# Kernel tuning notes

Hardware: AMD Instinct MI355X
Metric: run time of the kernel (lower is better)

Reference implementation:

```python
import jax, jax.numpy as jnp
import numpy as np

D = 256
NB = 12
B = 2
H = 800
W = 800
KS = [9, 9, 10, 11, 12, 13, 13, 14, 15, 16, 17, 18]
DILS = [1, 1, 1, 1, 2, 2, 2, 2, 3, 3, 3, 3]
STEM_CH = [3, D // 8, D // 4, D // 2, D, D]
STEM_STRIDE = [2, 2, 2, 2, 1]


def gelu(x):
    return jax.nn.gelu(x, approximate=False)


def conv3x3(x, w, b, stride):
    y = jax.lax.conv_general_dilated(x, w, (stride, stride), ((1, 1), (1, 1)),
                                     dimension_numbers=('NCHW', 'OIHW', 'NCHW'))
    return y + b[None, :, None, None]


def group_norm(x, g, be, groups=32, eps=1e-5):
    b, c, h, w = x.shape
    xg = x.reshape(b, groups, c // groups, h, w)
    m = xg.mean((2, 3, 4), keepdims=True)
    v = ((xg - m) ** 2).mean((2, 3, 4), keepdims=True)
    xg = (xg - m) * jax.lax.rsqrt(v + eps)
    return xg.reshape(b, c, h, w) * g[None, :, None, None] + be[None, :, None, None]


def pw(x, w, b, g, be):
    # 1x1 conv + eval-mode BatchNorm (running stats identity -> affine)
    y = jnp.einsum('oc,bcn->bon', w, x)
    if b is not None:
        y = y + b[None, :, None]
    return y * g[None, :, None] + be[None, :, None]


def pos_embed(b, c, h, w):
    # DETR-style normalized 2D sine position embedding -> [b, c, h, w]
    half = c // 2
    scale = 2.0 * np.pi
    ye = jnp.broadcast_to(jnp.arange(1, h + 1, dtype=jnp.float32)[:, None], (h, w)) / h * scale
    xe = jnp.broadcast_to(jnp.arange(1, w + 1, dtype=jnp.float32)[None, :], (h, w)) / w * scale
    dim_t = 10000.0 ** (2.0 * (jnp.arange(half) // 2).astype(jnp.float32) / half)
    px = xe[..., None] / dim_t
    py = ye[..., None] / dim_t
    px = jnp.stack([jnp.sin(px[..., 0::2]), jnp.cos(px[..., 1::2])], -1).reshape(h, w, half)
    py = jnp.stack([jnp.sin(py[..., 0::2]), jnp.cos(py[..., 1::2])], -1).reshape(h, w, half)
    pos = jnp.concatenate([py, px], -1).transpose(2, 0, 1)
    return jnp.broadcast_to(pos[None], (b, c, h, w))


def knn_graph(x, k, dil):
    # x: [B, C, N]; L2-normalize channels, neg squared dist, top-(k*dil), stride by dil
    xn = x * jax.lax.rsqrt(jnp.sum(x * x, 1, keepdims=True) + 1e-12)
    xt = xn.transpose(0, 2, 1)  # [B, N, C]
    sq = jnp.sum(xt * xt, -1)
    neg = 2.0 * jnp.einsum('bnc,bmc->bnm', xt, xt) - sq[:, :, None] - sq[:, None, :]
    _, idx = jax.lax.top_k(neg, k * dil)
    return idx[:, :, ::dil]  # [B, N, k]


def setup_inputs():
    key = jax.random.key(0)
    ks = jax.random.split(key, 16)
    inp = {"x": jax.random.normal(ks[0], (B, 3, H, W), jnp.float32)}
    for i in range(5):
        ci, co = STEM_CH[i], STEM_CH[i + 1]
        inp["sw%d" % i] = jax.random.normal(ks[1 + i], (co, ci, 3, 3), jnp.float32) * 0.05
        inp["sb%d" % i] = jnp.zeros((co,), jnp.float32)
        inp["sg%d" % i] = jnp.ones((co,), jnp.float32)
        inp["sbe%d" % i] = jnp.zeros((co,), jnp.float32)
    s = 0.02
    inp["fc1_w"] = jax.random.normal(ks[6], (NB, D, D), jnp.float32) * s
    inp["fc1_b"] = jnp.zeros((NB, D), jnp.float32)
    inp["fc1_g"] = jnp.ones((NB, D), jnp.float32)
    inp["fc1_be"] = jnp.zeros((NB, D), jnp.float32)
    inp["mr_w"] = jax.random.normal(ks[7], (NB, 2 * D, 2 * D), jnp.float32) * s
    inp["mr_g"] = jnp.ones((NB, 2 * D), jnp.float32)
    inp["mr_be"] = jnp.zeros((NB, 2 * D), jnp.float32)
    inp["fc2_w"] = jax.random.normal(ks[8], (NB, D, 2 * D), jnp.float32) * s
    inp["fc2_b"] = jnp.zeros((NB, D), jnp.float32)
    inp["fc2_g"] = jnp.ones((NB, D), jnp.float32)
    inp["fc2_be"] = jnp.zeros((NB, D), jnp.float32)
    inp["ffn1_w"] = jax.random.normal(ks[9], (NB, 4 * D, D), jnp.float32) * s
    inp["ffn1_b"] = jnp.zeros((NB, 4 * D), jnp.float32)
    inp["ffn1_g"] = jnp.ones((NB, 4 * D), jnp.float32)
    inp["ffn1_be"] = jnp.zeros((NB, 4 * D), jnp.float32)
    inp["ffn2_w"] = jax.random.normal(ks[10], (NB, D, 4 * D), jnp.float32) * s
    inp["ffn2_b"] = jnp.zeros((NB, D), jnp.float32)
    inp["ffn2_g"] = jnp.ones((NB, D), jnp.float32)
    inp["ffn2_be"] = jnp.zeros((NB, D), jnp.float32)
    return inp


def _forward(x, sw0, sb0, sg0, sbe0, sw1, sb1, sg1, sbe1, sw2, sb2, sg2, sbe2,
             sw3, sb3, sg3, sbe3, sw4, sb4, sg4, sbe4,
             fc1_w, fc1_b, fc1_g, fc1_be, mr_w, mr_g, mr_be,
             fc2_w, fc2_b, fc2_g, fc2_be, ffn1_w, ffn1_b, ffn1_g, ffn1_be,
             ffn2_w, ffn2_b, ffn2_g, ffn2_be):
    sws = [sw0, sw1, sw2, sw3, sw4]
    sbs = [sb0, sb1, sb2, sb3, sb4]
    sgs = [sg0, sg1, sg2, sg3, sg4]
    sbes = [sbe0, sbe1, sbe2, sbe3, sbe4]
    for i in range(5):
        x = conv3x3(x, sws[i], sbs[i], STEM_STRIDE[i])
        x = group_norm(x, sgs[i], sbes[i])
        if i < 4:
            x = gelu(x)
    b, c, h, w = x.shape
    x = x + pos_embed(b, c, h, w)
    n = h * w
    x = x.reshape(b, c, n)
    gather = jax.vmap(lambda t, ii: t[ii])  # ([N,C],[N,K]) -> [N,K,C], vmapped over batch
    for i in range(NB):
        # ---- Grapher block ----
        res = x
        hfeat = pw(x, fc1_w[i], fc1_b[i], fc1_g[i], fc1_be[i])  # [b, C, n]
        idx = knn_graph(hfeat, KS[i], DILS[i])                   # [b, n, k]
        ht = hfeat.transpose(0, 2, 1)                            # [b, n, C]
        xj = gather(ht, idx)                                     # [b, n, k, C]
        diff = jnp.max(xj - ht[:, :, None, :], axis=2)           # [b, n, C]
        # channel-interleaved concat: [x0, d0, x1, d1, ...]
        f = jnp.stack([ht, diff], -1).reshape(b, n, 2 * c).transpose(0, 2, 1)
        f = jnp.einsum('oc,bcn->bon', mr_w[i], f)
        f = gelu(f * mr_g[i][None, :, None] + mr_be[i][None, :, None])
        h2 = pw(f, fc2_w[i], fc2_b[i], fc2_g[i], fc2_be[i])
        x = h2 + res
        # ---- FFN block ----
        res = x
        hf = gelu(pw(x, ffn1_w[i], ffn1_b[i], ffn1_g[i], ffn1_be[i]))
        x = pw(hf, ffn2_w[i], ffn2_b[i], ffn2_g[i], ffn2_be[i]) + res
    return x.reshape(b, c, h, w)


def reference(x, sw0, sb0, sg0, sbe0, sw1, sb1, sg1, sbe1, sw2, sb2, sg2, sbe2,
              sw3, sb3, sg3, sbe3, sw4, sb4, sg4, sbe4,
              fc1_w, fc1_b, fc1_g, fc1_be, mr_w, mr_g, mr_be,
              fc2_w, fc2_b, fc2_g, fc2_be, ffn1_w, ffn1_b, ffn1_g, ffn1_be,
              ffn2_w, ffn2_b, ffn2_g, ffn2_be):
    return _forward(x, sw0, sb0, sg0, sbe0, sw1, sb1, sg1, sbe1, sw2, sb2, sg2, sbe2,
                    sw3, sb3, sg3, sbe3, sw4, sb4, sg4, sbe4,
                    fc1_w, fc1_b, fc1_g, fc1_be, mr_w, mr_g, mr_be,
                    fc2_w, fc2_b, fc2_g, fc2_be, ffn1_w, ffn1_b, ffn1_g, ffn1_be,
                    ffn2_w, ffn2_b, ffn2_g, ffn2_be)
```

## Files before the change

kernel.cpp:

```cpp
#include <hip/hip_runtime.h>
#include <math.h>

#define DEVI static __device__ __forceinline__

typedef __attribute__((ext_vector_type(8))) short short8b;
typedef __attribute__((ext_vector_type(4))) float f32x4;

DEVI float gelu_f(float x) { return 0.5f * x * (1.0f + erff(x * 0.70710678118654752440f)); }

DEVI unsigned pack2(float x)
{
    unsigned xb = __float_as_uint(x);
    unsigned hi = (xb + 0x7FFFu + ((xb >> 16) & 1u)) & 0xFFFF0000u;
    float lof = x - __uint_as_float(hi);
    unsigned lb = __float_as_uint(lof);
    unsigned lo = (lb + 0x7FFFu + ((lb >> 16) & 1u)) >> 16;
    return hi | lo;
}
DEVI float unpk(unsigned u)
{
    return __uint_as_float(u & 0xFFFF0000u) + __uint_as_float(u << 16);
}
DEVI unsigned bf16r(float x)
{
    unsigned b = __float_as_uint(x);
    return (b + 0x7FFFu + ((b >> 16) & 1u)) >> 16;
}
DEVI float bf2f(unsigned short u) { return __uint_as_float((unsigned)u << 16); }

DEVI short8b ldfrag(const unsigned* P, int row, int kq)
{
    const unsigned* b = P + row * 18 + kq * 2;
    union { uint2 h[2]; short8b s; } r;
    r.h[0] = *(const uint2*)(b);
    r.h[1] = *(const uint2*)(b + 8);
    return r.s;
}
DEVI void st8(unsigned* b, uint4 v0, uint4 v1)
{
    uint2 t;
    t.x = v0.x; t.y = v0.y; *(uint2*)(b) = t;
    t.x = v0.z; t.y = v0.w; *(uint2*)(b + 2) = t;
    t.x = v1.x; t.y = v1.y; *(uint2*)(b + 4) = t;
    t.x = v1.z; t.y = v1.w; *(uint2*)(b + 6) = t;
}
DEVI void st4(unsigned* b, uint4 v0)
{
    uint2 t;
    t.x = v0.x; t.y = v0.y; *(uint2*)(b) = t;
    t.x = v0.z; t.y = v0.w; *(uint2*)(b + 2) = t;
}

#define MFMA6(ACC, A0, A1, A2F, W0, W1, W2F) do { \
    ACC = __builtin_amdgcn_mfma_f32_16x16x32_bf16(A2F, W0, ACC, 0, 0, 0); \
    ACC = __builtin_amdgcn_mfma_f32_16x16x32_bf16(A0, W2F, ACC, 0, 0, 0); \
    ACC = __builtin_amdgcn_mfma_f32_16x16x32_bf16(A1, W1, ACC, 0, 0, 0); \
    ACC = __builtin_amdgcn_mfma_f32_16x16x32_bf16(A1, W0, ACC, 0, 0, 0); \
    ACC = __builtin_amdgcn_mfma_f32_16x16x32_bf16(A0, W1, ACC, 0, 0, 0); \
    ACC = __builtin_amdgcn_mfma_f32_16x16x32_bf16(A0, W0, ACC, 0, 0, 0); \
} while (0)

template <int CIN, int NCO>
__global__ __launch_bounds__(256)
void conv3x3_t(const float* __restrict__ in, const float* __restrict__ w,
               const float* __restrict__ bias, float* __restrict__ out,
               int Cout, int Hin, int Win, int Hout, int Wout, int stride)
{
    __shared__ __align__(16) float wlds[CIN * 9 * NCO];
    int nsx = gridDim.x, nco = gridDim.y;
    int fid = blockIdx.x + nsx * (blockIdx.y + nco * blockIdx.z);
    int S = nsx * gridDim.z;
    int sPer = S >> 3;
    int k8 = fid & 7, j = fid >> 3;
    int site_inst = k8 + 8 * (j % sPer);
    int co_g = j / sPer;
    int sx = site_inst % nsx;
    int b = site_inst / nsx;

    int co0 = co_g * NCO;
    int tid = threadIdx.x;
    int HWo = Hout * Wout;
    int s = sx * 256 + tid;
    int sc = (s < HWo) ? s : (HWo - 1);
    int ho = sc / Wout, wo = sc % Wout;
    float acc[NCO];
#pragma unroll
    for (int jj = 0; jj < NCO; jj++) acc[jj] = bias[co0 + jj];
    const float* inb = in + (size_t)b * CIN * Hin * Win;
    size_t HWi = (size_t)Hin * Win;

    const int nw = NCO * CIN * 9;
    for (int i = tid; i < nw; i += 256) {
        int jj = i % NCO;
        int rest = i / NCO;
        int ci = rest % CIN, tap = rest / CIN;
        wlds[i] = w[((size_t)(co0 + jj) * CIN + ci) * 9 + tap];
    }
    __syncthreads();
    for (int kh = 0; kh < 3; kh++) {
        int hi = ho * stride - 1 + kh;
        bool okh = (hi >= 0 && hi < Hin);
        for (int kw = 0; kw < 3; kw++) {
            int wi = wo * stride - 1 + kw;
            if (!okh || wi < 0 || wi >= Win) continue;
            int tap = kh * 3 + kw;
            const float* ip = inb + (size_t)hi * Win + wi;
            const float* wp = wlds + (size_t)tap * CIN * NCO;
#pragma unroll 4
            for (int ci = 0; ci < CIN; ci++) {
                float xv = ip[(size_t)ci * HWi];
                const float* wq = wp + ci * NCO;
#pragma unroll
                for (int j4 = 0; j4 < NCO; j4 += 4) {
                    float4 wv = *(const float4*)(wq + j4);
                    acc[j4 + 0] += xv * wv.x; acc[j4 + 1] += xv * wv.y;
                    acc[j4 + 2] += xv * wv.z; acc[j4 + 3] += xv * wv.w;
                }
            }
        }
    }
    if (s < HWo) {
        size_t ob = ((size_t)b * Cout + co0) * HWo + s;
#pragma unroll
        for (int jj = 0; jj < NCO; jj++) out[ob + (size_t)jj * HWo] = acc[jj];
    }
}

__global__ __launch_bounds__(256)
void gn_stats_k(const float* __restrict__ x, double* __restrict__ part,
                int C, int HW, int cpg, int S)
{
    int srt = blockIdx.x, g = blockIdx.y, b = blockIdx.z;
    long len = (long)cpg * HW;
    long chunk = (len + S - 1) / S;
    long lo = (long)srt * chunk;
    long hi = lo + chunk; if (hi > len) hi = len;
    const float* xp = x + ((size_t)b * C + (size_t)g * cpg) * HW;
    double s1 = 0.0, s2 = 0.0;
    for (long i = lo + threadIdx.x; i < hi; i += 256) {
        double v = (double)xp[i];
        s1 += v; s2 += v * v;
    }
    __shared__ double r1[256], r2[256];
    r1[threadIdx.x] = s1; r2[threadIdx.x] = s2;
    __syncthreads();
    for (int t = 128; t > 0; t >>= 1) {
        if (threadIdx.x < t) { r1[threadIdx.x] += r1[threadIdx.x + t]; r2[threadIdx.x] += r2[threadIdx.x + t]; }
        __syncthreads();
    }
    if (threadIdx.x == 0) {
        size_t slot = ((size_t)(b * 32 + g) * S + srt) * 2;
        part[slot] = r1[0];
        part[slot + 1] = r2[0];
    }
}

__global__ __launch_bounds__(64)
void gn_reduce_k(const double* __restrict__ part, float* __restrict__ fin,
                 int S, double cnt)
{
    int t = threadIdx.x;
    double s1 = 0.0, s2 = 0.0;
    for (int s = 0; s < S; s++) {
        size_t slot = ((size_t)t * S + s) * 2;
        s1 += part[slot];
        s2 += part[slot + 1];
    }
    double m = s1 / cnt;
    double var = s2 / cnt - m * m;
    double inv = 1.0 / sqrt(var + 1e-5);
    fin[t * 2] = (float)m;
    fin[t * 2 + 1] = (float)inv;
}

__global__ __launch_bounds__(256)
void gn_apply_k(float* __restrict__ x, const float* __restrict__ fin,
                const float* __restrict__ gma, const float* __restrict__ bta,
                int C, int HW, int cpg, int do_gelu, int total)
{
    int idx = blockIdx.x * 256 + threadIdx.x;
    if (idx >= total) return;
    int c = (idx / HW) % C;
    int b = idx / (HW * C);
    int g = c / cpg;
    float m = fin[(b * 32 + g) * 2];
    float inv = fin[(b * 32 + g) * 2 + 1];
    float v = (x[idx] - m) * inv * gma[c] + bta[c];
    if (do_gelu) v = gelu_f(v);
    x[idx] = v;
}

__global__ __launch_bounds__(256)
void splitT_k(const float* __restrict__ in, unsigned short* __restrict__ P0,
              unsigned short* __restrict__ P1, unsigned short* __restrict__ P2,
              int C, int HW)
{
    __shared__ float tile[64][65];
    int h0 = blockIdx.x * 64, c0 = blockIdx.y * 64, b = blockIdx.z;
    int tid = threadIdx.x;
    int tl = tid & 63;
    const float* inb = in + (size_t)b * C * HW;
#pragma unroll
    for (int p = 0; p < 16; p++) {
        int c = (tid >> 6) + p * 4;
        int h = h0 + tl;
        tile[c][tl] = (h < HW) ? inb[(size_t)(c0 + c) * HW + h] : 0.f;
    }
    __syncthreads();
#pragma unroll
    for (int p = 0; p < 16; p++) {
        int hh = (tid >> 6) + p * 4;
        int h = h0 + hh;
        if (h >= HW) continue;
        int ch = c0 + tl;
        float v = tile[tl][hh];
        unsigned pm = pack2(v);
        size_t off = ((size_t)b * HW + h) * C + ch;
        P0[off] = (unsigned short)(pm >> 16);
        P1[off] = (unsigned short)(pm & 0xFFFFu);
        P2[off] = (unsigned short)bf16r(v - unpk(pm));
    }
}

__global__ __launch_bounds__(256)
void wconvp_k(const float* __restrict__ w, unsigned short* __restrict__ P0,
              unsigned short* __restrict__ P1, unsigned short* __restrict__ P2,
              int Cin, int total)
{
    int idx = blockIdx.x * 256 + threadIdx.x;
    if (idx >= total) return;
    int K = Cin * 9;
    int co = idx / K, k = idx % K;
    int tap = k / Cin, ci = k - tap * Cin;
    float v = w[((size_t)co * Cin + ci) * 9 + tap];
    unsigned pm = pack2(v);
    P0[idx] = (unsigned short)(pm >> 16);
    P1[idx] = (unsigned short)(pm & 0xFFFFu);
    P2[idx] = (unsigned short)bf16r(v - unpk(pm));
}

__global__ __launch_bounds__(256)
void pack5p_k(const float* __restrict__ s0, const float* __restrict__ s1,
              const float* __restrict__ s2, const float* __restrict__ s3,
              const float* __restrict__ s4, unsigned short* __restrict__ P0,
              unsigned short* __restrict__ P1, unsigned short* __restrict__ P2)
{
    int idx = blockIdx.x * 256 + threadIdx.x;
    float v;
    if (idx < 65536)       v = s0[idx];
    else if (idx < 327680) v = s1[idx - 65536];
    else if (idx < 458752) v = s2[idx - 327680];
    else if (idx < 720896) v = s3[idx - 458752];
    else                   v = s4[idx - 720896];
    unsigned pm = pack2(v);
    P0[idx] = (unsigned short)(pm >> 16);
    P1[idx] = (unsigned short)(pm & 0xFFFFu);
    P2[idx] = (unsigned short)bf16r(v - unpk(pm));
}

template <int JT>
__global__ __launch_bounds__(256, 3)
void mgemm6p_k(const unsigned short* __restrict__ A0, const unsigned short* __restrict__ A1,
               const unsigned short* __restrict__ A2,
               const unsigned short* __restrict__ W0, const unsigned short* __restrict__ W1,
               const unsigned short* __restrict__ W2,
               const float* __restrict__ bias, const float* __restrict__ gma,
               const float* __restrict__ bta,
               const unsigned short* __restrict__ R0, const unsigned short* __restrict__ R1,
               const unsigned short* __restrict__ R2,
               unsigned short* __restrict__ C0, unsigned short* __restrict__ C1,
               unsigned short* __restrict__ C2,
               int N, int M, int K, int do_gelu)
{
    const int BM = 32 * JT;
    __shared__ __align__(16) unsigned lA[3][64 * 18];
    __shared__ __align__(16) unsigned lW[3][BM * 18];
    int bz = blockIdx.z;
    int n0 = blockIdx.x * 64, m0 = blockIdx.y * BM;
    int tid = threadIdx.x, wave = tid >> 6, lane = tid & 63;
    int wn = (wave & 1) * 32, wm = (wave >> 1) * (16 * JT);
    int rl = lane & 15, kq = lane >> 4;

    f32x4 acc[2][JT] = {};

    const unsigned* Ag[3] = {(const unsigned*)A0, (const unsigned*)A1, (const unsigned*)A2};
    const unsigned* Wg[3] = {(const unsigned*)W0, (const unsigned*)W1, (const unsigned*)W2};

    int ar = tid >> 2, ah = tid & 3;
    int aga = n0 + ar; if (aga >= N) aga = N - 1;
    size_t abase = (((size_t)bz * N + aga) * K) >> 1;
    unsigned* sA[3];
#pragma unroll
    for (int pl = 0; pl < 3; pl++) sA[pl] = &lA[pl][ar * 18 + ah * 4];

    int wr_ = (JT == 4) ? (tid >> 1) : (tid >> 2);
    int wo_ = (JT == 4) ? ((tid & 1) * 8) : ((tid & 3) * 4);
    size_t wbase = ((size_t)(m0 + wr_) * K) >> 1;
    unsigned* sW[3];
#pragma unroll
    for (int pl = 0; pl < 3; pl++) sW[pl] = &lW[pl][wr_ * 18 + wo_];

    uint4 pa[3], pw[3][2];

#pragma unroll
    for (int pl = 0; pl < 3; pl++) {
        pa[pl] = *(const uint4*)(Ag[pl] + abase + ah * 4);
        const unsigned* h = Wg[pl] + wbase + wo_;
        pw[pl][0] = *(const uint4*)(h);
        if (JT == 4) pw[pl][1] = *(const uint4*)(h + 4);
    }
#pragma unroll
    for (int pl = 0; pl < 3; pl++) {
        st4(sA[pl], pa[pl]);
        if (JT == 4) st8(sW[pl], pw[pl][0], pw[pl][1]); else st4(sW[pl], pw[pl][0]);
    }
    __syncthreads();

    for (int k0 = 0; k0 < K; k0 += 32) {
        bool more = (k0 + 32) < K;
        if (more) {
#pragma unroll
            for (int pl = 0; pl < 3; pl++) {
                pa[pl] = *(const uint4*)(Ag[pl] + abase + ((k0 + 32) >> 1) + ah * 4);
                const unsigned* h = Wg[pl] + wbase + ((k0 + 32) >> 1) + wo_;
                pw[pl][0] = *(const uint4*)(h);
                if (JT == 4) pw[pl][1] = *(const uint4*)(h + 4);
            }
        }
        short8b a0[2], a1[2], a2[2];
#pragma unroll
        for (int i = 0; i < 2; i++) {
            int ra = wn + i * 16 + rl;
            a0[i] = ldfrag(lA[0], ra, kq);
            a1[i] = ldfrag(lA[1], ra, kq);
            a2[i] = ldfrag(lA[2], ra, kq);
        }
        short8b w0[JT], w1[JT], w2[JT];
#pragma unroll
        for (int j = 0; j < JT; j++) {
            int rw = wm + j * 16 + rl;
            w0[j] = ldfrag(lW[0], rw, kq);
            w1[j] = ldfrag(lW[1], rw, kq);
            w2[j] = ldfrag(lW[2], rw, kq);
        }
#pragma unroll
        for (int i = 0; i < 2; i++) {
#pragma unroll
            for (int j = 0; j < JT; j++) {
                MFMA6(acc[i][j], a0[i], a1[i], a2[i], w0[j], w1[j], w2[j]);
            }
        }
        __syncthreads();
        if (more) {
#pragma unroll
            for (int pl = 0; pl < 3; pl++) {
                st4(sA[pl], pa[pl]);
                if (JT == 4) st8(sW[pl], pw[pl][0], pw[pl][1]); else st4(sW[pl], pw[pl][0]);
            }
            __syncthreads();
        }
    }

#pragma unroll
    for (int j = 0; j < JT; j++) {
        int mm = m0 + wm + j * 16 + rl;
        float bs = bias ? bias[mm] : 0.f;
        float gm = gma[mm], bt = bta[mm];
#pragma unroll
        for (int i = 0; i < 2; i++) {
            int tn = n0 + wn + i * 16 + kq * 4;
            f32x4 a = acc[i][j];
#pragma unroll
            for (int r = 0; r < 4; r++) {
                int gn2 = tn + r;
                if (gn2 >= N) continue;
                float v = (a[r] + bs) * gm + bt;
                if (do_gelu) v = gelu_f(v);
                size_t off = ((size_t)bz * N + gn2) * M + mm;
                if (R0) v += (bf2f(R0[off]) + bf2f(R1[off])) + bf2f(R2[off]);
                unsigned pm = pack2(v);
                C0[off] = (unsigned short)(pm >> 16);
                C1[off] = (unsigned short)(pm & 0xFFFFu);
                C2[off] = (unsigned short)bf16r(v - unpk(pm));
            }
        }
    }
}

__global__ __launch_bounds__(256, 3)
void mdist6p_k(const unsigned short* __restrict__ H0, const unsigned short* __restrict__ H1,
               const unsigned short* __restrict__ H2, const float* __restrict__ SQ,
               float* __restrict__ NEG, int Nn, int K, int bz)
{
    __shared__ __align__(16) unsigned lA[3][64 * 18];
    __shared__ __align__(16) unsigned lW[3][64 * 18];
    int q = blockIdx.x;
    int ti = 0;
    while (q >= 40 - ti) { q -= 40 - ti; ti++; }
    int tj = ti + q;
    int i0 = ti * 64, j0 = tj * 64;
    int tid = threadIdx.x, wave = tid >> 6, lane = tid & 63;
    int wn = (wave & 1) * 32, wm = (wave >> 1) * 32;
    int rl = lane & 15, kq = lane >> 4;

    f32x4 acc[2][2] = {};

    const unsigned* Hg[3] = {(const unsigned*)H0, (const unsigned*)H1, (const unsigned*)H2};

    int ar = tid >> 2, ah = tid & 3;
    int gi = i0 + ar; if (gi >= Nn) gi = Nn - 1;
    int gj = j0 + ar; if (gj >= Nn) gj = Nn - 1;
    size_t ibase = (((size_t)bz * Nn + gi) * K) >> 1;
    size_t jbase = (((size_t)bz * Nn + gj) * K) >> 1;
    unsigned* sA[3];
    unsigned* sW[3];
#pragma unroll
    for (int pl = 0; pl < 3; pl++) {
        sA[pl] = &lA[pl][ar * 18 + ah * 4];
        sW[pl] = &lW[pl][ar * 18 + ah * 4];
    }

    uint4 pa[3], pj[3];
#pragma unroll
    for (int pl = 0; pl < 3; pl++) {
        pa[pl] = *(const uint4*)(Hg[pl] + ibase + ah * 4);
        pj[pl] = *(const uint4*)(Hg[pl] + jbase + ah * 4);
    }
#pragma unroll
    for (int pl = 0; pl < 3; pl++) {
        st4(sA[pl], pa[pl]);
        st4(sW[pl], pj[pl]);
    }
    __syncthreads();

    for (int k0 = 0; k0 < K; k0 += 32) {
        bool more = (k0 + 32) < K;
        if (more) {
#pragma unroll
            for (int pl = 0; pl < 3; pl++) {
                pa[pl] = *(const uint4*)(Hg[pl] + ibase + ((k0 + 32) >> 1) + ah * 4);
                pj[pl] = *(const uint4*)(Hg[pl] + jbase + ((k0 + 32) >> 1) + ah * 4);
            }
        }
        short8b a0[2], a1[2], a2[2], w0[2], w1[2], w2[2];
#pragma unroll
        for (int i = 0; i < 2; i++) {
            int ra = wn + i * 16 + rl;
            a0[i] = ldfrag(lA[0], ra, kq);
            a1[i] = ldfrag(lA[1], ra, kq);
            a2[i] = ldfrag(lA[2], ra, kq);
            int rw = wm + i * 16 + rl;
            w0[i] = ldfrag(lW[0], rw, kq);
            w1[i] = ldfrag(lW[1], rw, kq);
            w2[i] = ldfrag(lW[2], rw, kq);
        }
#pragma unroll
        for (int i = 0; i < 2; i++) {
#pragma unroll
            for (int j = 0; j < 2; j++) {
                MFMA6(acc[i][j], a0[i], a1[i], a2[i], w0[j], w1[j], w2[j]);
            }
        }
        __syncthreads();
        if (more) {
#pragma unroll
            for (int pl = 0; pl < 3; pl++) {
                st4(sA[pl], pa[pl]);
                st4(sW[pl], pj[pl]);
            }
            __syncthreads();
        }
    }

    const float* SQb = SQ + (size_t)bz * Nn;
#pragma unroll
    for (int j = 0; j < 2; j++) {
        int nj = j0 + wm + j * 16 + rl;
        if (nj >= Nn) continue;
        float sj = SQb[nj];
#pragma unroll
        for (int i = 0; i < 2; i++) {
            int nio = i0 + wn + i * 16 + kq * 4;
            f32x4 a = acc[i][j];
#pragma unroll
            for (int r = 0; r < 4; r++) {
                int ni = nio + r;
                if (ni >= Nn) continue;
                float d = 2.f * a[r] - SQb[ni] - sj;
                NEG[(size_t)ni * Nn + nj] = d;
                if (i0 != j0) NEG[(size_t)nj * Nn + ni] = d;
            }
        }
    }
}

template <int CIN>
__global__ __launch_bounds__(256, 3)
void mconv6p_k(const unsigned short* __restrict__ T0, const unsigned short* __restrict__ T1,
               const unsigned short* __restrict__ T2,
               const unsigned short* __restrict__ Wc0, const unsigned short* __restrict__ Wc1,
               const unsigned short* __restrict__ Wc2,
               const float* __restrict__ bias, float* __restrict__ out,
               int Cout, int Hin, int Win, int Hout, int Wout, int stride)
{
    const int K = 9 * CIN;
    __shared__ __align__(16) unsigned lA[3][64 * 18];
    __shared__ __align__(16) unsigned lW[3][64 * 18];
    int bz = blockIdx.z;
    int n0 = blockIdx.x * 64, m0 = blockIdx.y * 64;
    int HWo = Hout * Wout;
    int tid = threadIdx.x, wave = tid >> 6, lane = tid & 63;
    int wn = (wave & 1) * 32, wm = (wave >> 1) * 32;
    int rl = lane & 15, kq = lane >> 4;

    f32x4 acc[2][2] = {};

    const unsigned* Tg[3] = {(const unsigned*)T0, (const unsigned*)T1, (const unsigned*)T2};
    const unsigned* Wg[3] = {(const unsigned*)Wc0, (const unsigned*)Wc1, (const unsigned*)Wc2};

    int ar = tid >> 2, ah = tid & 3;
    int s = n0 + ar; if (s >= HWo) s = HWo - 1;
    int ho = s / Wout, wo = s % Wout;
    unsigned* sA[3];
#pragma unroll
    for (int pl = 0; pl < 3; pl++) sA[pl] = &lA[pl][ar * 18 + ah * 4];

    int wr_ = tid >> 2, wo_ = (tid & 3) * 4;
    size_t wbase = ((size_t)(m0 + wr_) * K) >> 1;
    unsigned* sW[3];
#pragma unroll
    for (int pl = 0; pl < 3; pl++) sW[pl] = &lW[pl][wr_ * 18 + wo_];
    size_t HWi = (size_t)Hin * Win;

    uint4 pa[3], pw[3];

    auto loadS = [&](int ks) {
        int kk = ks * 32;
        int tap = kk / CIN;
        int kh = tap / 3, kw = tap % 3;
        int hi = ho * stride - 1 + kh;
        int wi = wo * stride - 1 + kw;
        bool ok = (hi >= 0 && hi < Hin && wi >= 0 && wi < Win);
        if (ok) {
            size_t base = (((size_t)bz * HWi + (size_t)(hi * Win + wi)) * CIN + (kk % CIN)) >> 1;
#pragma unroll
            for (int pl = 0; pl < 3; pl++)
                pa[pl] = *(const uint4*)(Tg[pl] + base + ah * 4);
        } else {
            uint4 z; z.x = 0; z.y = 0; z.z = 0; z.w = 0;
#pragma unroll
            for (int pl = 0; pl < 3; pl++) pa[pl] = z;
        }
#pragma unroll
        for (int pl = 0; pl < 3; pl++)
            pw[pl] = *(const uint4*)(Wg[pl] + wbase + ks * 16 + wo_);
    };
    auto stS = [&]() {
#pragma unroll
        for (int pl = 0; pl < 3; pl++) {
            st4(sA[pl], pa[pl]);
            st4(sW[pl], pw[pl]);
        }
    };

    int nst = K >> 5;
    loadS(0);
    stS();
    __syncthreads();

    for (int ks = 0; ks < nst; ks++) {
        bool more = (ks + 1) < nst;
        if (more) loadS(ks + 1);
        short8b a0[2], a1[2], a2[2];
#pragma unroll
        for (int i = 0; i < 2; i++) {
            int ra = wn + i * 16 + rl;
            a0[i] = ldfrag(lA[0], ra, kq);
            a1[i] = ldfrag(lA[1], ra, kq);
            a2[i] = ldfrag(lA[2], ra, kq);
        }
        short8b w0[2], w1[2], w2[2];
#pragma unroll
        for (int j = 0; j < 2; j++) {
            int rw = wm + j * 16 + rl;
            w0[j] = ldfrag(lW[0], rw, kq);
            w1[j] = ldfrag(lW[1], rw, kq);
            w2[j] = ldfrag(lW[2], rw, kq);
        }
#pragma unroll
        for (int i = 0; i < 2; i++) {
#pragma unroll
            for (int j = 0; j < 2; j++) {
                MFMA6(acc[i][j], a0[i], a1[i], a2[i], w0[j], w1[j], w2[j]);
            }
        }
        __syncthreads();
        if (more) {
            stS();
            __syncthreads();
        }
    }

#pragma unroll
    for (int j = 0; j < 2; j++) {
        int mm = m0 + wm + j * 16 + rl;
        float bs = bias[mm];
#pragma unroll
        for (int i = 0; i < 2; i++) {
            int tn = n0 + wn + i * 16 + kq * 4;
            f32x4 a = acc[i][j];
#pragma unroll
            for (int r = 0; r < 4; r++) {
                int gn2 = tn + r;
                if (gn2 < HWo)
                    out[((size_t)bz * Cout + mm) * HWo + gn2] = a[r] + bs;
            }
        }
    }
}

__global__ __launch_bounds__(256)
void posadd_k(const float* __restrict__ xin, unsigned short* __restrict__ X0,
              unsigned short* __restrict__ X1, unsigned short* __restrict__ X2)
{
    __shared__ float tile[64][65];
    int t0 = blockIdx.x * 64, c0 = blockIdx.y * 64, b = blockIdx.z;
    int tid = threadIdx.x;
    int tl = tid & 63;
    const float* inb = xin + (size_t)b * 256 * 2500;
#pragma unroll
    for (int p = 0; p < 16; p++) {
        int c = (tid >> 6) + p * 4;
        int t = t0 + tl;
        tile[c][tl] = (t < 2500) ? inb[(size_t)(c0 + c) * 2500 + t] : 0.f;
    }
    __syncthreads();
#pragma unroll
    for (int p = 0; p < 16; p++) {
        int tt = (tid >> 6) + p * 4;
        int t = t0 + tt;
        if (t >= 2500) continue;
        int ch = c0 + tl;
        int yy = t / 50, xx = t % 50;
        int cc = ch & 127;
        double v = (double)((ch < 128) ? (yy + 1) : (xx + 1));
        v = v * (6.283185307179586476925287 / 50.0);
        double e = (double)(2 * (cc >> 1)) / 128.0;
        double d = pow(10000.0, e);
        double a = v / d;
        double pp = (cc & 1) ? cos(a) : sin(a);
        float val = tile[tl][tt] + (float)pp;
        size_t off = ((size_t)b * 2500 + t) * 256 + ch;
        unsigned pm = pack2(val);
        X0[off] = (unsigned short)(pm >> 16);
        X1[off] = (unsigned short)(pm & 0xFFFFu);
        X2[off] = (unsigned short)bf16r(val - unpk(pm));
    }
}

__global__ __launch_bounds__(256)
void tok_k(const unsigned short* __restrict__ H0, const unsigned short* __restrict__ H1,
           const unsigned short* __restrict__ H2, unsigned short* __restrict__ T0,
           unsigned short* __restrict__ T1, unsigned short* __restrict__ T2,
           float* __restrict__ SQ)
{
    int wave = threadIdx.x >> 6, lane = threadIdx.x & 63;
    int t = blockIdx.x * 4 + wave;
    int b = blockIdx.y;
    size_t base = ((size_t)b * 2500 + t) * 128;
    const unsigned* h0 = (const unsigned*)H0 + base;
    const unsigned* h1 = (const unsigned*)H1 + base;
    const unsigned* h2 = (const unsigned*)H2 + base;
    float v[4];
    double s = 0.0;
#pragma unroll
    for (int g = 0; g < 2; g++) {
        unsigned ua = h0[lane + g * 64], ub = h1[lane + g * 64], uc = h2[lane + g * 64];
        float lo = (__uint_as_float(ua << 16) + __uint_as_float(ub << 16)) + __uint_as_float(uc << 16);
        float hi = (__uint_as_float(ua & 0xFFFF0000u) + __uint_as_float(ub & 0xFFFF0000u)) + __uint_as_float(uc & 0xFFFF0000u);
        v[2 * g] = lo; v[2 * g + 1] = hi;
        s += (double)lo * lo + (double)hi * hi;
    }
#pragma unroll
    for (int off = 32; off > 0; off >>= 1) s += __shfl_xor(s, off);
    float r = (float)(1.0 / sqrt(s + 1e-12));
    unsigned* t0 = (unsigned*)T0 + base;
    unsigned* t1 = (unsigned*)T1 + base;
    unsigned* t2 = (unsigned*)T2 + base;
    double s2 = 0.0;
#pragma unroll
    for (int g = 0; g < 2; g++) {
        float x0 = v[2 * g] * r, x1 = v[2 * g + 1] * r;
        s2 += (double)x0 * x0 + (double)x1 * x1;
        unsigned p0 = pack2(x0), p1 = pack2(x1);
        t0[lane + g * 64] = (p0 >> 16) | (p1 & 0xFFFF0000u);
        t1[lane + g * 64] = (p0 & 0xFFFFu) | (p1 << 16);
        t2[lane + g * 64] = bf16r(x0 - unpk(p0)) | (bf16r(x1 - unpk(p1)) << 16);
    }
#pragma unroll
    for (int off = 32; off > 0; off >>= 1) s2 += __shfl_xor(s2, off);
    if (lane == 0) SQ[b * 2500 + t] = (float)s2;
}

DEVI unsigned long long pack_key(float x, unsigned idx)
{
    unsigned u = __float_as_uint(x);
    u = (u & 0x80000000u) ? ~u : (u | 0x80000000u);
    return ((unsigned long long)u << 32) | (unsigned long long)(0xFFFFFFFFu - idx);
}

__global__ __launch_bounds__(128)
void topk_k(const float* __restrict__ NEGc, int* __restrict__ IDX,
            int rows, int kd, int dil, int kout, int bz)
{
    __shared__ float vals[2][2560];
    int wave = threadIdx.x >> 6;
    int lane = threadIdx.x & 63;
    int i = blockIdx.x * 2 + wave;
    if (i >= rows) return;
    const float* row = NEGc + (size_t)i * 2500;
    float* v = vals[wave];
    for (int j = lane; j < 2560; j += 64)
        v[j] = (j < 2500) ? (row[j] + 0.0f) : -INFINITY;
    unsigned long long key = pack_key(-INFINITY, 0xFFFFFFFFu);
    for (int q = 0; q < 40; q++) {
        int pos = lane * 40 + q;
        unsigned long long k2 = pack_key(v[pos], (unsigned)pos);
        if (k2 > key) key = k2;
    }
    for (int t = 0; t < kd; t++) {
        unsigned long long r = key;
#pragma unroll
        for (int off = 32; off > 0; off >>= 1) {
            unsigned long long o = __shfl_xor(r, off);
            if (o > r) r = o;
        }
        int sel = (int)(0xFFFFFFFFu - (unsigned)(r & 0xFFFFFFFFull));
        if ((unsigned)sel >= 2500u) sel = 0;
        if (lane == 0 && t % dil == 0)
            IDX[(size_t)(bz * 2500 + i) * kout + t / dil] = sel;
        int lo = sel / 40;
        if (lane == lo) v[sel] = -INFINITY;
        int pos = lo * 40 + lane;
        float x = (lane < 40) ? v[pos] : -INFINITY;
        unsigned long long k2 = pack_key(x, (lane < 40) ? (unsigned)pos : 0xFFFFFFFFu);
#pragma unroll
        for (int off = 32; off > 0; off >>= 1) {
            unsigned long long o = __shfl_xor(k2, off);
            if (o > k2) k2 = o;
        }
        if (lane == lo) key = k2;
    }
}

__global__ __launch_bounds__(256)
void gather_k(const unsigned short* __restrict__ H0, const unsigned short* __restrict__ H1,
              const unsigned short* __restrict__ H2, const int* __restrict__ IDX,
              unsigned short* __restrict__ F0, unsigned short* __restrict__ F1,
              unsigned short* __restrict__ F2, int k)
{
    int t = blockIdx.x;
    int b = blockIdx.y;
    int q = threadIdx.x;
    __shared__ int idx[18];
    if (q < k) {
        int ii = IDX[((size_t)b * 2500 + t) * k + q];
        if ((unsigned)ii >= 2500u) ii = 0;
        idx[q] = ii;
    }
    __syncthreads();
    size_t base = (size_t)b * 2500 * 256;
    size_t co = base + (size_t)t * 256 + q;
    float center = (bf2f(H0[co]) + bf2f(H1[co])) + bf2f(H2[co]);
    float mx = -INFINITY;
    for (int kk = 0; kk < k; kk++) {
        size_t no = base + (size_t)idx[kk] * 256 + q;
        float v = (bf2f(H0[no]) + bf2f(H1[no])) + bf2f(H2[no]);
        mx = fmaxf(mx, v - center);
    }
    unsigned pc = pack2(center), pd = pack2(mx);
    size_t fo = (size_t)b * 2500 * 256 + (size_t)t * 256 + q;
    ((unsigned*)F0)[fo] = (pc >> 16) | (pd & 0xFFFF0000u);
    ((unsigned*)F1)[fo] = (pc & 0xFFFFu) | (pd << 16);
    ((unsigned*)F2)[fo] = bf16r(center - unpk(pc)) | (bf16r(mx - unpk(pd)) << 16);
}

__global__ __launch_bounds__(256)
void outt_k(const unsigned short* __restrict__ X0, const unsigned short* __restrict__ X1,
            const unsigned short* __restrict__ X2, float* __restrict__ out)
{
    __shared__ float tile[64][65];
    int t0 = blockIdx.x * 64, c0 = blockIdx.y * 64, b = blockIdx.z;
    int tid = threadIdx.x;
    int tl = tid & 63;
#pragma unroll
    for (int p = 0; p < 16; p++) {
        int tt = (tid >> 6) + p * 4;
        int t = t0 + tt;
        int tc = (t < 2500) ? t : 2499;
        size_t off = ((size_t)b * 2500 + tc) * 256 + c0 + tl;
        tile[tl][tt] = (bf2f(X0[off]) + bf2f(X1[off])) + bf2f(X2[off]);
    }
    __syncthreads();
#pragma unroll
    for (int p = 0; p < 16; p++) {
        int cc = (tid >> 6) + p * 4;
        int t = t0 + tl;
        if (t < 2500)
            out[((size_t)b * 256 + c0 + cc) * 2500 + t] = tile[cc][tl];
    }
}

extern "C" void kernel_launch(void* const* d_in, const int* in_sizes, int n_in,
                              void* d_out, int out_size, void* d_ws, size_t ws_size,
                              hipStream_t stream)
{
    (void)in_sizes; (void)n_in; (void)out_size; (void)ws_size;
    const float* x_in = (const float*)d_in[0];
    const float *swp[5], *sbp[5], *sgp[5], *sbep[5];
    for (int i = 0; i < 5; i++) {
        swp[i] = (const float*)d_in[1 + 4 * i];
        sbp[i] = (const float*)d_in[2 + 4 * i];
        sgp[i] = (const float*)d_in[3 + 4 * i];
        sbep[i] = (const float*)d_in[4 + 4 * i];
    }
    const float* fc1_w = (const float*)d_in[21];
    const float* fc1_b = (const float*)d_in[22];
    const float* fc1_g = (const float*)d_in[23];
    const float* fc1_be = (const float*)d_in[24];
    const float* mr_w = (const float*)d_in[25];
    const float* mr_g = (const float*)d_in[26];
    const float* mr_be = (const float*)d_in[27];
    const float* fc2_w = (const float*)d_in[28];
    const float* fc2_b = (const float*)d_in[29];
    const float* fc2_g = (const float*)d_in[30];
    const float* fc2_be = (const float*)d_in[31];
    const float* ffn1_w = (const float*)d_in[32];
    const float* ffn1_b = (const float*)d_in[33];
    const float* ffn1_g = (const float*)d_in[34];
    const float* ffn1_be = (const float*)d_in[35];
    const float* ffn2_w = (const float*)d_in[36];
    const float* ffn2_b = (const float*)d_in[37];
    const float* ffn2_g = (const float*)d_in[38];
    const float* ffn2_be = (const float*)d_in[39];

    float* ws = (float*)d_ws;
    const size_t NEG_F = 1920000;
    const size_t G_F   = 3840000;
    const size_t TI_F  = 3000000;
    const size_t CW_F  = 10300000;
    const size_t X_F   = 12500000;
    const size_t HF_F  = 14420000;
    const size_t W_F   = 16340000;
    const size_t SQ_F  = 17815000;
    const size_t PART_F = 17820000;
    const size_t FIN_F = 17829000;
    const size_t IDX_F = 17830000;

    float* ping = ws;
    float* pong = ws + X_F;
    float* NEG  = ws + NEG_F;
    unsigned short* HT0 = (unsigned short*)ws;
    unsigned short* HT1 = HT0 + 1280000;
    unsigned short* HT2 = HT0 + 2560000;
    unsigned short* Fp0 = (unsigned short*)ws;
    unsigned short* Fp1 = Fp0 + 2560000;
    unsigned short* Fp2 = Fp0 + 5120000;
    unsigned short* Gp0 = (unsigned short*)(ws + G_F);
    unsigned short* Gp1 = Gp0 + 2560000;
    unsigned short* Gp2 = Gp0 + 5120000;
    unsigned short* H20 = (unsigned short*)ws;
    unsigned short* H21 = H20 + 5120000;
    unsigned short* H22 = H20 + 10240000;
    unsigned short* TI0 = (unsigned short*)(ws + TI_F);
    unsigned short* CW0 = (unsigned short*)(ws + CW_F);
    unsigned short* X0 = (unsigned short*)(ws + X_F);
    unsigned short* X1 = X0 + 1280000;
    unsigned short* X2 = X0 + 2560000;
    unsigned short* HF0 = (unsigned short*)(ws + HF_F);
    unsigned short* HF1 = HF0 + 1280000;
    unsigned short* HF2b = HF0 + 2560000;
    unsigned short* W0 = (unsigned short*)(ws + W_F);
    unsigned short* W1 = W0 + 983040;
    unsigned short* W2 = W0 + 1966080;
    float* SQ = ws + SQ_F;
    double* PART = (double*)(ws + PART_F);
    float* FIN = ws + FIN_F;
    int* IDX = (int*)(ws + IDX_F);

    int Co[5] = {32, 64, 128, 256, 256};
    int Ho[5] = {400, 200, 100, 50, 50};
    int Ssub[5] = {8, 8, 4, 2, 2};
    float* cur = nullptr;
    for (int l = 0; l < 5; l++) {
        float* outb = (l % 2 == 0) ? ping : pong;
        int HWo = Ho[l] * Ho[l];
        switch (l) {
        case 0:
            conv3x3_t<3, 32><<<dim3(628, 1, 2), 256, 0, stream>>>(
                x_in, swp[0], sbp[0], outb, 32, 800, 800, 400, 400, 2);
            break;
        case 1:
            conv3x3_t<32, 32><<<dim3(160, 2, 2), 256, 0, stream>>>(
                cur, swp[1], sbp[1], outb, 64, 400, 400, 200, 200, 2);
            break;
        case 2:
            conv3x3_t<64, 16><<<dim3(40, 8, 2), 256, 0, stream>>>(
                cur, swp[2], sbp[2], outb, 128, 200, 200, 100, 100, 2);
            break;
        case 3: {
            int psz = 2 * 10000 * 128;
            splitT_k<<<dim3(157, 2, 2), 256, 0, stream>>>(
                cur, TI0, TI0 + psz, TI0 + 2 * psz, 128, 10000);
            int tot = 256 * 1152;
            wconvp_k<<<(tot + 255) / 256, 256, 0, stream>>>(
                swp[3], CW0, CW0 + tot, CW0 + 2 * tot, 128, tot);
            mconv6p_k<128><<<dim3(40, 4, 2), 256, 0, stream>>>(
                TI0, TI0 + psz, TI0 + 2 * psz, CW0, CW0 + tot, CW0 + 2 * tot,
                sbp[3], outb, 256, 100, 100, 50, 50, 2);
            break;
        }
        case 4: {
            int psz = 2 * 2500 * 256;
            splitT_k<<<dim3(40, 4, 2), 256, 0, stream>>>(
                cur, TI0, TI0 + psz, TI0 + 2 * psz, 256, 2500);
            int tot = 256 * 2304;
            wconvp_k<<<(tot + 255) / 256, 256, 0, stream>>>(
                swp[4], CW0, CW0 + tot, CW0 + 2 * tot, 256, tot);
            mconv6p_k<256><<<dim3(40, 4, 2), 256, 0, stream>>>(
                TI0, TI0 + psz, TI0 + 2 * psz, CW0, CW0 + tot, CW0 + 2 * tot,
                sbp[4], outb, 256, 50, 50, 50, 50, 1);
            break;
        }
        }
        int cpg = Co[l] / 32;
        gn_stats_k<<<dim3(Ssub[l], 32, 2), 256, 0, stream>>>(outb, PART, Co[l], HWo, cpg, Ssub[l]);
        gn_reduce_k<<<1, 64, 0, stream>>>(PART, FIN, Ssub[l], (double)cpg * (double)HWo);
        int total = 2 * Co[l] * HWo;
        gn_apply_k<<<(total + 255) / 256, 256, 0, stream>>>(outb, FIN, sgp[l], sbep[l],
                                                            Co[l], HWo, cpg, (l < 4) ? 1 : 0, total);
        cur = outb;
    }
    posadd_k<<<dim3(40, 4, 2), 256, 0, stream>>>(cur, X0, X1, X2);

    const int KS[12] = {9, 9, 10, 11, 12, 13, 13, 14, 15, 16, 17, 18};
    const int DILS[12] = {1, 1, 1, 1, 2, 2, 2, 2, 3, 3, 3, 3};
    const int D = 256, N = 2500;

    for (int i = 0; i < 12; i++) {
        pack5p_k<<<3840, 256, 0, stream>>>(
            fc1_w + (size_t)i * 65536, mr_w + (size_t)i * 262144,
            fc2_w + (size_t)i * 131072, ffn1_w + (size_t)i * 262144,
            ffn2_w + (size_t)i * 262144, W0, W1, W2);

        mgemm6p_k<2><<<dim3(40, 4, 2), 256, 0, stream>>>(
            X0, X1, X2, W0, W1, W2,
            fc1_b + i * D, fc1_g + i * D, fc1_be + i * D,
            nullptr, nullptr, nullptr, HF0, HF1, HF2b, N, D, D, 0);
        tok_k<<<dim3(625, 2), 256, 0, stream>>>(HF0, HF1, HF2b, HT0, HT1, HT2, SQ);
        for (int bz = 0; bz < 2; bz++) {
            mdist6p_k<<<dim3(820, 1, 1), 256, 0, stream>>>(HT0, HT1, HT2, SQ, NEG, N, D, bz);
            topk_k<<<dim3(1250, 1, 1), 128, 0, stream>>>(NEG, IDX, N,
                                                         KS[i] * DILS[i], DILS[i], KS[i], bz);
        }
        gather_k<<<dim3(2500, 2), 256, 0, stream>>>(HF0, HF1, HF2b, IDX, Fp0, Fp1, Fp2, KS[i]);
        mgemm6p_k<4><<<dim3(40, 4, 2), 256, 0, stream>>>(
            Fp0, Fp1, Fp2, W0 + 65536, W1 + 65536, W2 + 65536,
            nullptr, mr_g + i * 512, mr_be + i * 512,
            nullptr, nullptr, nullptr, Gp0, Gp1, Gp2, N, 512, 512, 1);
        mgemm6p_k<2><<<dim3(40, 4, 2), 256, 0, stream>>>(
            Gp0, Gp1, Gp2, W0 + 327680, W1 + 327680, W2 + 327680,
            fc2_b + i * D, fc2_g + i * D, fc2_be + i * D,
            X0, X1, X2, X0, X1, X2, N, D, 512, 0);
        mgemm6p_k<4><<<dim3(40, 8, 2), 256, 0, stream>>>(
            X0, X1, X2, W0 + 458752, W1 + 458752, W2 + 458752,
            ffn1_b + i * 1024, ffn1_g + i * 1024, ffn1_be + i * 1024,
            nullptr, nullptr, nullptr, H20, H21, H22, N, 1024, D, 1);
        mgemm6p_k<2><<<dim3(40, 4, 2), 256, 0, stream>>>(
            H20, H21, H22, W0 + 720896, W1 + 720896, W2 + 720896,
            ffn2_b + i * D, ffn2_g + i * D, ffn2_be + i * D,
            X0, X1, X2, X0, X1, X2, N, D, 1024, 0);
    }

    outt_k<<<dim3(40, 4, 2), 256, 0, stream>>>(X0, X1, X2, (float*)d_out);
}
```

Baseline: 4.390 ms.

## Replace 3-way bf16 split emulation with 2-way fp16 split MFMA

Switches the fp32-emulating matmul scheme from three bf16 planes with six MFMAs per tile to two fp16 planes (hi + residual) with three f16 MFMAs per tile, across the GEMM, distance and conv kernels, and the pack/gather/output helpers. This roughly halves MFMA count, LDS footprint and the global traffic for the split activations and weights. The trade-off is numerical: fp16 has limited exponent range, so large or tiny values may overflow or lose precision, and this could change kNN selection.

```diff
diff --git a/kernel.cpp b/kernel.cpp
--- a/kernel.cpp
+++ b/kernel.cpp
@@ -3,38 +3,34 @@
 
 #define DEVI static __device__ __forceinline__
 
-typedef __attribute__((ext_vector_type(8))) short short8b;
+typedef __attribute__((ext_vector_type(8))) _Float16 half8;
 typedef __attribute__((ext_vector_type(4))) float f32x4;
 
 DEVI float gelu_f(float x) { return 0.5f * x * (1.0f + erff(x * 0.70710678118654752440f)); }
 
-DEVI unsigned pack2(float x)
-{
-    unsigned xb = __float_as_uint(x);
-    unsigned hi = (xb + 0x7FFFu + ((xb >> 16) & 1u)) & 0xFFFF0000u;
-    float lof = x - __uint_as_float(hi);
-    unsigned lb = __float_as_uint(lof);
-    unsigned lo = (lb + 0x7FFFu + ((lb >> 16) & 1u)) >> 16;
-    return hi | lo;
-}
-DEVI float unpk(unsigned u)
-{
-    return __uint_as_float(u & 0xFFFF0000u) + __uint_as_float(u << 16);
-}
-DEVI unsigned bf16r(float x)
-{
-    unsigned b = __float_as_uint(x);
-    return (b + 0x7FFFu + ((b >> 16) & 1u)) >> 16;
-}
-DEVI float bf2f(unsigned short u) { return __uint_as_float((unsigned)u << 16); }
-
-DEVI short8b ldfrag(const unsigned* P, int row, int kq)
+DEVI unsigned short f2h(float x)
+{
+    _Float16 h = (_Float16)x;
+    unsigned short u; __builtin_memcpy(&u, &h, 2); return u;
+}
+DEVI float h2f(unsigned short u)
+{
+    _Float16 h; __builtin_memcpy(&h, &u, 2); return (float)h;
+}
+
+DEVI half8 ldfh(const unsigned* P, int row, int kq)
 {
     const unsigned* b = P + row * 18 + kq * 2;
-    union { uint2 h[2]; short8b s; } r;
+    union { uint2 h[2]; half8 s; } r;
     r.h[0] = *(const uint2*)(b);
     r.h[1] = *(const uint2*)(b + 8);
     return r.s;
+}
+DEVI void st4(unsigned* b, uint4 v0)
+{
+    uint2 t;
+    t.x = v0.x; t.y = v0.y; *(uint2*)(b) = t;
+    t.x = v0.z; t.y = v0.w; *(uint2*)(b + 2) = t;
 }
 DEVI void st8(unsigned* b, uint4 v0, uint4 v1)
 {
@@ -44,20 +40,11 @@
     t.x = v1.x; t.y = v1.y; *(uint2*)(b + 4) = t;
     t.x = v1.z; t.y = v1.w; *(uint2*)(b + 6) = t;
 }
-DEVI void st4(unsigned* b, uint4 v0)
-{
-    uint2 t;
-    t.x = v0.x; t.y = v0.y; *(uint2*)(b) = t;
-    t.x = v0.z; t.y = v0.w; *(uint2*)(b + 2) = t;
-}
-
-#define MFMA6(ACC, A0, A1, A2F, W0, W1, W2F) do { \
-    ACC = __builtin_amdgcn_mfma_f32_16x16x32_bf16(A2F, W0, ACC, 0, 0, 0); \
-    ACC = __builtin_amdgcn_mfma_f32_16x16x32_bf16(A0, W2F, ACC, 0, 0, 0); \
-    ACC = __builtin_amdgcn_mfma_f32_16x16x32_bf16(A1, W1, ACC, 0, 0, 0); \
-    ACC = __builtin_amdgcn_mfma_f32_16x16x32_bf16(A1, W0, ACC, 0, 0, 0); \
-    ACC = __builtin_amdgcn_mfma_f32_16x16x32_bf16(A0, W1, ACC, 0, 0, 0); \
-    ACC = __builtin_amdgcn_mfma_f32_16x16x32_bf16(A0, W0, ACC, 0, 0, 0); \
+
+#define MFMA3(ACC, A0, A1, W0, W1) do { \
+    ACC = __builtin_amdgcn_mfma_f32_16x16x32_f16(A1, W0, ACC, 0, 0, 0); \
+    ACC = __builtin_amdgcn_mfma_f32_16x16x32_f16(A0, W1, ACC, 0, 0, 0); \
+    ACC = __builtin_amdgcn_mfma_f32_16x16x32_f16(A0, W0, ACC, 0, 0, 0); \
 } while (0)
 
 template <int CIN, int NCO>
@@ -192,8 +179,7 @@
 
 __global__ __launch_bounds__(256)
 void splitT_k(const float* __restrict__ in, unsigned short* __restrict__ P0,
-              unsigned short* __restrict__ P1, unsigned short* __restrict__ P2,
-              int C, int HW)
+              unsigned short* __restrict__ P1, int C, int HW)
 {
     __shared__ float tile[64][65];
     int h0 = blockIdx.x * 64, c0 = blockIdx.y * 64, b = blockIdx.z;
@@ -214,18 +200,16 @@
         if (h >= HW) continue;
         int ch = c0 + tl;
         float v = tile[tl][hh];
-        unsigned pm = pack2(v);
+        unsigned short a = f2h(v);
         size_t off = ((size_t)b * HW + h) * C + ch;
-        P0[off] = (unsigned short)(pm >> 16);
-        P1[off] = (unsigned short)(pm & 0xFFFFu);
-        P2[off] = (unsigned short)bf16r(v - unpk(pm));
+        P0[off] = a;
+        P1[off] = f2h(v - h2f(a));
     }
 }
 
 __global__ __launch_bounds__(256)
 void wconvp_k(const float* __restrict__ w, unsigned short* __restrict__ P0,
-              unsigned short* __restrict__ P1, unsigned short* __restrict__ P2,
-              int Cin, int total)
+              unsigned short* __restrict__ P1, int Cin, int total)
 {
     int idx = blockIdx.x * 256 + threadIdx.x;
     if (idx >= total) return;
@@ -233,17 +217,16 @@
     int co = idx / K, k = idx % K;
     int tap = k / Cin, ci = k - tap * Cin;
     float v = w[((size_t)co * Cin + ci) * 9 + tap];
-    unsigned pm = pack2(v);
-    P0[idx] = (unsigned short)(pm >> 16);
-    P1[idx] = (unsigned short)(pm & 0xFFFFu);
-    P2[idx] = (unsigned short)bf16r(v - unpk(pm));
+    unsigned short a = f2h(v);
+    P0[idx] = a;
+    P1[idx] = f2h(v - h2f(a));
 }
 
 __global__ __launch_bounds__(256)
 void pack5p_k(const float* __restrict__ s0, const float* __restrict__ s1,
               const float* __restrict__ s2, const float* __restrict__ s3,
               const float* __restrict__ s4, unsigned short* __restrict__ P0,
-              unsigned short* __restrict__ P1, unsigned short* __restrict__ P2)
+              unsigned short* __restrict__ P1)
 {
     int idx = blockIdx.x * 256 + threadIdx.x;
     float v;
@@ -252,29 +235,24 @@
     else if (idx < 458752) v = s2[idx - 327680];
     else if (idx < 720896) v = s3[idx - 458752];
     else                   v = s4[idx - 720896];
-    unsigned pm = pack2(v);
-    P0[idx] = (unsigned short)(pm >> 16);
-    P1[idx] = (unsigned short)(pm & 0xFFFFu);
-    P2[idx] = (unsigned short)bf16r(v - unpk(pm));
+    unsigned short a = f2h(v);
+    P0[idx] = a;
+    P1[idx] = f2h(v - h2f(a));
 }
 
 template <int JT>
 __global__ __launch_bounds__(256, 3)
-void mgemm6p_k(const unsigned short* __restrict__ A0, const unsigned short* __restrict__ A1,
-               const unsigned short* __restrict__ A2,
+void mgemm3h_k(const unsigned short* __restrict__ A0, const unsigned short* __restrict__ A1,
                const unsigned short* __restrict__ W0, const unsigned short* __restrict__ W1,
-               const unsigned short* __restrict__ W2,
                const float* __restrict__ bias, const float* __restrict__ gma,
                const float* __restrict__ bta,
                const unsigned short* __restrict__ R0, const unsigned short* __restrict__ R1,
-               const unsigned short* __restrict__ R2,
                unsigned short* __restrict__ C0, unsigned short* __restrict__ C1,
-               unsigned short* __restrict__ C2,
                int N, int M, int K, int do_gelu)
 {
     const int BM = 32 * JT;
-    __shared__ __align__(16) unsigned lA[3][64 * 18];
-    __shared__ __align__(16) unsigned lW[3][BM * 18];
+    __shared__ __align__(16) unsigned lA[2][64 * 18];
+    __shared__ __align__(16) unsigned lW[2][BM * 18];
     int bz = blockIdx.z;
     int n0 = blockIdx.x * 64, m0 = blockIdx.y * BM;
     int tid = threadIdx.x, wave = tid >> 6, lane = tid & 63;
@@ -283,34 +261,34 @@
 
     f32x4 acc[2][JT] = {};
 
-    const unsigned* Ag[3] = {(const unsigned*)A0, (const unsigned*)A1, (const unsigned*)A2};
-    const unsigned* Wg[3] = {(const unsigned*)W0, (const unsigned*)W1, (const unsigned*)W2};
+    const unsigned* Ag[2] = {(const unsigned*)A0, (const unsigned*)A1};
+    const unsigned* Wg[2] = {(const unsigned*)W0, (const unsigned*)W1};
 
     int ar = tid >> 2, ah = tid & 3;
     int aga = n0 + ar; if (aga >= N) aga = N - 1;
     size_t abase = (((size_t)bz * N + aga) * K) >> 1;
-    unsigned* sA[3];
-#pragma unroll
-    for (int pl = 0; pl < 3; pl++) sA[pl] = &lA[pl][ar * 18 + ah * 4];
+    unsigned* sA[2];
+#pragma unroll
+    for (int pl = 0; pl < 2; pl++) sA[pl] = &lA[pl][ar * 18 + ah * 4];
 
     int wr_ = (JT == 4) ? (tid >> 1) : (tid >> 2);
     int wo_ = (JT == 4) ? ((tid & 1) * 8) : ((tid & 3) * 4);
     size_t wbase = ((size_t)(m0 + wr_) * K) >> 1;
-    unsigned* sW[3];
-#pragma unroll
-    for (int pl = 0; pl < 3; pl++) sW[pl] = &lW[pl][wr_ * 18 + wo_];
-
-    uint4 pa[3], pw[3][2];
-
-#pragma unroll
-    for (int pl = 0; pl < 3; pl++) {
+    unsigned* sW[2];
+#pragma unroll
+    for (int pl = 0; pl < 2; pl++) sW[pl] = &lW[pl][wr_ * 18 + wo_];
+
+    uint4 pa[2], pw[2][2];
+
+#pragma unroll
+    for (int pl = 0; pl < 2; pl++) {
         pa[pl] = *(const uint4*)(Ag[pl] + abase + ah * 4);
         const unsigned* h = Wg[pl] + wbase + wo_;
         pw[pl][0] = *(const uint4*)(h);
         if (JT == 4) pw[pl][1] = *(const uint4*)(h + 4);
     }
 #pragma unroll
-    for (int pl = 0; pl < 3; pl++) {
+    for (int pl = 0; pl < 2; pl++) {
         st4(sA[pl], pa[pl]);
         if (JT == 4) st8(sW[pl], pw[pl][0], pw[pl][1]); else st4(sW[pl], pw[pl][0]);
     }
@@ -320,40 +298,38 @@
         bool more = (k0 + 32) < K;
         if (more) {
 #pragma unroll
-            for (int pl = 0; pl < 3; pl++) {
+            for (int pl = 0; pl < 2; pl++) {
                 pa[pl] = *(const uint4*)(Ag[pl] + abase + ((k0 + 32) >> 1) + ah * 4);
                 const unsigned* h = Wg[pl] + wbase + ((k0 + 32) >> 1) + wo_;
                 pw[pl][0] = *(const uint4*)(h);
                 if (JT == 4) pw[pl][1] = *(const uint4*)(h + 4);
             }
         }
-        short8b a0[2], a1[2], a2[2];
+        half8 a0[2], a1[2];
 #pragma unroll
         for (int i = 0; i < 2; i++) {
             int ra = wn + i * 16 + rl;
-            a0[i] = ldfrag(lA[0], ra, kq);
-            a1[i] = ldfrag(lA[1], ra, kq);
-            a2[i] = ldfrag(lA[2], ra, kq);
-        }
-        short8b w0[JT], w1[JT], w2[JT];
+            a0[i] = ldfh(lA[0], ra, kq);
+            a1[i] = ldfh(lA[1], ra, kq);
+        }
+        half8 w0[JT], w1[JT];
 #pragma unroll
         for (int j = 0; j < JT; j++) {
             int rw = wm + j * 16 + rl;
-            w0[j] = ldfrag(lW[0], rw, kq);
-            w1[j] = ldfrag(lW[1], rw, kq);
-            w2[j] = ldfrag(lW[2], rw, kq);
+            w0[j] = ldfh(lW[0], rw, kq);
+            w1[j] = ldfh(lW[1], rw, kq);
         }
 #pragma unroll
         for (int i = 0; i < 2; i++) {
 #pragma unroll
             for (int j = 0; j < JT; j++) {
-                MFMA6(acc[i][j], a0[i], a1[i], a2[i], w0[j], w1[j], w2[j]);
+                MFMA3(acc[i][j], a0[i], a1[i], w0[j], w1[j]);
             }
         }
         __syncthreads();
         if (more) {
 #pragma unroll
-            for (int pl = 0; pl < 3; pl++) {
+            for (int pl = 0; pl < 2; pl++) {
                 st4(sA[pl], pa[pl]);
                 if (JT == 4) st8(sW[pl], pw[pl][0], pw[pl][1]); else st4(sW[pl], pw[pl][0]);
             }
@@ -377,23 +353,22 @@
                 float v = (a[r] + bs) * gm + bt;
                 if (do_gelu) v = gelu_f(v);
                 size_t off = ((size_t)bz * N + gn2) * M + mm;
-                if (R0) v += (bf2f(R0[off]) + bf2f(R1[off])) + bf2f(R2[off]);
-                unsigned pm = pack2(v);
-                C0[off] = (unsigned short)(pm >> 16);
-                C1[off] = (unsigned short)(pm & 0xFFFFu);
-                C2[off] = (unsigned short)bf16r(v - unpk(pm));
+                if (R0) v += h2f(R0[off]) + h2f(R1[off]);
+                unsigned short c0 = f2h(v);
+                C0[off] = c0;
+                C1[off] = f2h(v - h2f(c0));
             }
         }
     }
 }
 
 __global__ __launch_bounds__(256, 3)
-void mdist6p_k(const unsigned short* __restrict__ H0, const unsigned short* __restrict__ H1,
-               const unsigned short* __restrict__ H2, const float* __restrict__ SQ,
-               float* __restrict__ NEG, int Nn, int K, int bz)
-{
-    __shared__ __align__(16) unsigned lA[3][64 * 18];
-    __shared__ __align__(16) unsigned lW[3][64 * 18];
+void mdist3h_k(const unsigned short* __restrict__ H0, const unsigned short* __restrict__ H1,
+               const float* __restrict__ SQ, float* __restrict__ NEG,
+               int Nn, int K, int bz)
+{
+    __shared__ __align__(16) unsigned lA[2][64 * 18];
+    __shared__ __align__(16) unsigned lW[2][64 * 18];
     int q = blockIdx.x;
     int ti = 0;
     while (q >= 40 - ti) { q -= 40 - ti; ti++; }
@@ -405,29 +380,29 @@
 
     f32x4 acc[2][2] = {};
 
-    const unsigned* Hg[3] = {(const unsigned*)H0, (const unsigned*)H1, (const unsigned*)H2};
+    const unsigned* Hg[2] = {(const unsigned*)H0, (const unsigned*)H1};
 
     int ar = tid >> 2, ah = tid & 3;
     int gi = i0 + ar; if (gi >= Nn) gi = Nn - 1;
     int gj = j0 + ar; if (gj >= Nn) gj = Nn - 1;
     size_t ibase = (((size_t)bz * Nn + gi) * K) >> 1;
     size_t jbase = (((size_t)bz * Nn + gj) * K) >> 1;
-    unsigned* sA[3];
-    unsigned* sW[3];
-#pragma unroll
-    for (int pl = 0; pl < 3; pl++) {
+    unsigned* sA[2];
+    unsigned* sW[2];
+#pragma unroll
+    for (int pl = 0; pl < 2; pl++) {
         sA[pl] = &lA[pl][ar * 18 + ah * 4];
         sW[pl] = &lW[pl][ar * 18 + ah * 4];
     }
 
-    uint4 pa[3], pj[3];
-#pragma unroll
-    for (int pl = 0; pl < 3; pl++) {
+    uint4 pa[2], pj[2];
+#pragma unroll
+    for (int pl = 0; pl < 2; pl++) {
         pa[pl] = *(const uint4*)(Hg[pl] + ibase + ah * 4);
         pj[pl] = *(const uint4*)(Hg[pl] + jbase + ah * 4);
     }
 #pragma unroll
-    for (int pl = 0; pl < 3; pl++) {
+    for (int pl = 0; pl < 2; pl++) {
         st4(sA[pl], pa[pl]);
         st4(sW[pl], pj[pl]);
     }
@@ -437,34 +412,32 @@
         bool more = (k0 + 32) < K;
         if (more) {
 #pragma unroll
-            for (int pl = 0; pl < 3; pl++) {
+            for (int pl = 0; pl < 2; pl++) {
                 pa[pl] = *(const uint4*)(Hg[pl] + ibase + ((k0 + 32) >> 1) + ah * 4);
                 pj[pl] = *(const uint4*)(Hg[pl] + jbase + ((k0 + 32) >> 1) + ah * 4);
             }
         }
-        short8b a0[2], a1[2], a2[2], w0[2], w1[2], w2[2];
+        half8 a0[2], a1[2], w0[2], w1[2];
 #pragma unroll
         for (int i = 0; i < 2; i++) {
             int ra = wn + i * 16 + rl;
-            a0[i] = ldfrag(lA[0], ra, kq);
-            a1[i] = ldfrag(lA[1], ra, kq);
-            a2[i] = ldfrag(lA[2], ra, kq);
+            a0[i] = ldfh(lA[0], ra, kq);
+            a1[i] = ldfh(lA[1], ra, kq);
             int rw = wm + i * 16 + rl;
-            w0[i] = ldfrag(lW[0], rw, kq);
-            w1[i] = ldfrag(lW[1], rw, kq);
-            w2[i] = ldfrag(lW[2], rw, kq);
+            w0[i] = ldfh(lW[0], rw, kq);
+            w1[i] = ldfh(lW[1], rw, kq);
         }
 #pragma unroll
         for (int i = 0; i < 2; i++) {
 #pragma unroll
             for (int j = 0; j < 2; j++) {
-                MFMA6(acc[i][j], a0[i], a1[i], a2[i], w0[j], w1[j], w2[j]);
+                MFMA3(acc[i][j], a0[i], a1[i], w0[j], w1[j]);
             }
         }
         __syncthreads();
         if (more) {
 #pragma unroll
-            for (int pl = 0; pl < 3; pl++) {
+            for (int pl = 0; pl < 2; pl++) {
                 st4(sA[pl], pa[pl]);
                 st4(sW[pl], pj[pl]);
             }
@@ -496,16 +469,14 @@
 
 template <int CIN>
 __global__ __launch_bounds__(256, 3)
-void mconv6p_k(const unsigned short* __restrict__ T0, const unsigned short* __restrict__ T1,
-               const unsigned short* __restrict__ T2,
+void mconv3h_k(const unsigned short* __restrict__ T0, const unsigned short* __restrict__ T1,
                const unsigned short* __restrict__ Wc0, const unsigned short* __restrict__ Wc1,
-               const unsigned short* __restrict__ Wc2,
                const float* __restrict__ bias, float* __restrict__ out,
                int Cout, int Hin, int Win, int Hout, int Wout, int stride)
 {
     const int K = 9 * CIN;
-    __shared__ __align__(16) unsigned lA[3][64 * 18];
-    __shared__ __align__(16) unsigned lW[3][64 * 18];
+    __shared__ __align__(16) unsigned lA[2][64 * 18];
+    __shared__ __align__(16) unsigned lW[2][64 * 18];
     int bz = blockIdx.z;
     int n0 = blockIdx.x * 64, m0 = blockIdx.y * 64;
     int HWo = Hout * Wout;
@@ -515,24 +486,24 @@
 
     f32x4 acc[2][2] = {};
 
-    const unsigned* Tg[3] = {(const unsigned*)T0, (const unsigned*)T1, (const unsigned*)T2};
-    const unsigned* Wg[3] = {(const unsigned*)Wc0, (const unsigned*)Wc1, (const unsigned*)Wc2};
+    const unsigned* Tg[2] = {(const unsigned*)T0, (const unsigned*)T1};
+    const unsigned* Wg[2] = {(const unsigned*)Wc0, (const unsigned*)Wc1};
 
     int ar = tid >> 2, ah = tid & 3;
     int s = n0 + ar; if (s >= HWo) s = HWo - 1;
     int ho = s / Wout, wo = s % Wout;
-    unsigned* sA[3];
-#pragma unroll
-    for (int pl = 0; pl < 3; pl++) sA[pl] = &lA[pl][ar * 18 + ah * 4];
+    unsigned* sA[2];
+#pragma unroll
+    for (int pl = 0; pl < 2; pl++) sA[pl] = &lA[pl][ar * 18 + ah * 4];
 
     int wr_ = tid >> 2, wo_ = (tid & 3) * 4;
     size_t wbase = ((size_t)(m0 + wr_) * K) >> 1;
-    unsigned* sW[3];
-#pragma unroll
-    for (int pl = 0; pl < 3; pl++) sW[pl] = &lW[pl][wr_ * 18 + wo_];
+    unsigned* sW[2];
+#pragma unroll
+    for (int pl = 0; pl < 2; pl++) sW[pl] = &lW[pl][wr_ * 18 + wo_];
     size_t HWi = (size_t)Hin * Win;
 
-    uint4 pa[3], pw[3];
+    uint4 pa[2], pw[2];
 
     auto loadS = [&](int ks) {
         int kk = ks * 32;
@@ -544,20 +515,20 @@
         if (ok) {
             size_t base = (((size_t)bz * HWi + (size_t)(hi * Win + wi)) * CIN + (kk % CIN)) >> 1;
 #pragma unroll
-            for (int pl = 0; pl < 3; pl++)
+            for (int pl = 0; pl < 2; pl++)
                 pa[pl] = *(const uint4*)(Tg[pl] + base + ah * 4);
         } else {
             uint4 z; z.x = 0; z.y = 0; z.z = 0; z.w = 0;
 #pragma unroll
-            for (int pl = 0; pl < 3; pl++) pa[pl] = z;
-        }
-#pragma unroll
-        for (int pl = 0; pl < 3; pl++)
+            for (int pl = 0; pl < 2; pl++) pa[pl] = z;
+        }
+#pragma unroll
+        for (int pl = 0; pl < 2; pl++)
             pw[pl] = *(const uint4*)(Wg[pl] + wbase + ks * 16 + wo_);
     };
     auto stS = [&]() {
 #pragma unroll
-        for (int pl = 0; pl < 3; pl++) {
+        for (int pl = 0; pl < 2; pl++) {
             st4(sA[pl], pa[pl]);
             st4(sW[pl], pw[pl]);
         }
@@ -571,27 +542,25 @@
     for (int ks = 0; ks < nst; ks++) {
         bool more = (ks + 1) < nst;
         if (more) loadS(ks + 1);
-        short8b a0[2], a1[2], a2[2];
+        half8 a0[2], a1[2];
 #pragma unroll
         for (int i = 0; i < 2; i++) {
             int ra = wn + i * 16 + rl;
-            a0[i] = ldfrag(lA[0], ra, kq);
-            a1[i] = ldfrag(lA[1], ra, kq);
-            a2[i] = ldfrag(lA[2], ra, kq);
-        }
-        short8b w0[2], w1[2], w2[2];
+            a0[i] = ldfh(lA[0], ra, kq);
+            a1[i] = ldfh(lA[1], ra, kq);
+        }
+        half8 w0[2], w1[2];
 #pragma unroll
         for (int j = 0; j < 2; j++) {
             int rw = wm + j * 16 + rl;
-            w0[j] = ldfrag(lW[0], rw, kq);
-            w1[j] = ldfrag(lW[1], rw, kq);
-            w2[j] = ldfrag(lW[2], rw, kq);
+            w0[j] = ldfh(lW[0], rw, kq);
+            w1[j] = ldfh(lW[1], rw, kq);
         }
 #pragma unroll
         for (int i = 0; i < 2; i++) {
 #pragma unroll
             for (int j = 0; j < 2; j++) {
-                MFMA6(acc[i][j], a0[i], a1[i], a2[i], w0[j], w1[j], w2[j]);
+                MFMA3(acc[i][j], a0[i], a1[i], w0[j], w1[j]);
             }
         }
         __syncthreads();
@@ -621,7 +590,7 @@
 
 __global__ __launch_bounds__(256)
 void posadd_k(const float* __restrict__ xin, unsigned short* __restrict__ X0,
-              unsigned short* __restrict__ X1, unsigned short* __restrict__ X2)
+              unsigned short* __restrict__ X1)
 {
     __shared__ float tile[64][65];
     int t0 = blockIdx.x * 64, c0 = blockIdx.y * 64, b = blockIdx.z;
@@ -651,17 +620,15 @@
         double pp = (cc & 1) ? cos(a) : sin(a);
         float val = tile[tl][tt] + (float)pp;
         size_t off = ((size_t)b * 2500 + t) * 256 + ch;
-        unsigned pm = pack2(val);
-        X0[off] = (unsigned short)(pm >> 16);
-        X1[off] = (unsigned short)(pm & 0xFFFFu);
-        X2[off] = (unsigned short)bf16r(val - unpk(pm));
+        unsigned short a0 = f2h(val);
+        X0[off] = a0;
+        X1[off] = f2h(val - h2f(a0));
     }
 }
 
 __global__ __launch_bounds__(256)
 void tok_k(const unsigned short* __restrict__ H0, const unsigned short* __restrict__ H1,
-           const unsigned short* __restrict__ H2, unsigned short* __restrict__ T0,
-           unsigned short* __restrict__ T1, unsigned short* __restrict__ T2,
+           unsigned short* __restrict__ T0, unsigned short* __restrict__ T1,
            float* __restrict__ SQ)
 {
     int wave = threadIdx.x >> 6, lane = threadIdx.x & 63;
@@ -670,14 +637,13 @@
     size_t base = ((size_t)b * 2500 + t) * 128;
     const unsigned* h0 = (const unsigned*)H0 + base;
     const unsigned* h1 = (const unsigned*)H1 + base;
-    const unsigned* h2 = (const unsigned*)H2 + base;
     float v[4];
     double s = 0.0;
 #pragma unroll
     for (int g = 0; g < 2; g++) {
-        unsigned ua = h0[lane + g * 64], ub = h1[lane + g * 64], uc = h2[lane + g * 64];
-        float lo = (__uint_as_float(ua << 16) + __uint_as_float(ub << 16)) + __uint_as_float(uc << 16);
-        float hi = (__uint_as_float(ua & 0xFFFF0000u) + __uint_as_float(ub & 0xFFFF0000u)) + __uint_as_float(uc & 0xFFFF0000u);
+        unsigned ua = h0[lane + g * 64], ub = h1[lane + g * 64];
+        float lo = h2f((unsigned short)(ua & 0xFFFFu)) + h2f((unsigned short)(ub & 0xFFFFu));
+        float hi = h2f((unsigned short)(ua >> 16)) + h2f((unsigned short)(ub >> 16));
         v[2 * g] = lo; v[2 * g + 1] = hi;
         s += (double)lo * lo + (double)hi * hi;
     }
@@ -686,16 +652,15 @@
     float r = (float)(1.0 / sqrt(s + 1e-12));
     unsigned* t0 = (unsigned*)T0 + base;
     unsigned* t1 = (unsigned*)T1 + base;
-    unsigned* t2 = (unsigned*)T2 + base;
     double s2 = 0.0;
 #pragma unroll
     for (int g = 0; g < 2; g++) {
         float x0 = v[2 * g] * r, x1 = v[2 * g + 1] * r;
         s2 += (double)x0 * x0 + (double)x1 * x1;
-        unsigned p0 = pack2(x0), p1 = pack2(x1);
-        t0[lane + g * 64] = (p0 >> 16) | (p1 & 0xFFFF0000u);
-        t1[lane + g * 64] = (p0 & 0xFFFFu) | (p1 << 16);
-        t2[lane + g * 64] = bf16r(x0 - unpk(p0)) | (bf16r(x1 - unpk(p1)) << 16);
+        unsigned short a0 = f2h(x0), b0 = f2h(x1);
+        unsigned short a1 = f2h(x0 - h2f(a0)), b1 = f2h(x1 - h2f(b0));
+        t0[lane + g * 64] = (unsigned)a0 | ((unsigned)b0 << 16);
+        t1[lane + g * 64] = (unsigned)a1 | ((unsigned)b1 << 16);
     }
 #pragma unroll
     for (int off = 32; off > 0; off >>= 1) s2 += __shfl_xor(s2, off);
@@ -755,9 +720,8 @@
 
 __global__ __launch_bounds__(256)
 void gather_k(const unsigned short* __restrict__ H0, const unsigned short* __restrict__ H1,
-              const unsigned short* __restrict__ H2, const int* __restrict__ IDX,
-              unsigned short* __restrict__ F0, unsigned short* __restrict__ F1,
-              unsigned short* __restrict__ F2, int k)
+              const int* __restrict__ IDX,
+              unsigned short* __restrict__ F0, unsigned short* __restrict__ F1, int k)
 {
     int t = blockIdx.x;
     int b = blockIdx.y;
@@ -771,23 +735,23 @@
     __syncthreads();
     size_t base = (size_t)b * 2500 * 256;
     size_t co = base + (size_t)t * 256 + q;
-    float center = (bf2f(H0[co]) + bf2f(H1[co])) + bf2f(H2[co]);
+    float center = h2f(H0[co]) + h2f(H1[co]);
     float mx = -INFINITY;
     for (int kk = 0; kk < k; kk++) {
         size_t no = base + (size_t)idx[kk] * 256 + q;
-        float v = (bf2f(H0[no]) + bf2f(H1[no])) + bf2f(H2[no]);
+        float v = h2f(H0[no]) + h2f(H1[no]);
         mx = fmaxf(mx, v - center);
     }
-    unsigned pc = pack2(center), pd = pack2(mx);
+    unsigned short c0 = f2h(center), d0 = f2h(mx);
+    unsigned short c1 = f2h(center - h2f(c0)), d1 = f2h(mx - h2f(d0));
     size_t fo = (size_t)b * 2500 * 256 + (size_t)t * 256 + q;
-    ((unsigned*)F0)[fo] = (pc >> 16) | (pd & 0xFFFF0000u);
-    ((unsigned*)F1)[fo] = (pc & 0xFFFFu) | (pd << 16);
-    ((unsigned*)F2)[fo] = bf16r(center - unpk(pc)) | (bf16r(mx - unpk(pd)) << 16);
+    ((unsigned*)F0)[fo] = (unsigned)c0 | ((unsigned)d0 << 16);
+    ((unsigned*)F1)[fo] = (unsigned)c1 | ((unsigned)d1 << 16);
 }
 
 __global__ __launch_bounds__(256)
 void outt_k(const unsigned short* __restrict__ X0, const unsigned short* __restrict__ X1,
-            const unsigned short* __restrict__ X2, float* __restrict__ out)
+            float* __restrict__ out)
 {
     __shared__ float tile[64][65];
     int t0 = blockIdx.x * 64, c0 = blockIdx.y * 64, b = blockIdx.z;
@@ -799,7 +763,7 @@
         int t = t0 + tt;
         int tc = (t < 2500) ? t : 2499;
         size_t off = ((size_t)b * 2500 + tc) * 256 + c0 + tl;
-        tile[tl][tt] = (bf2f(X0[off]) + bf2f(X1[off])) + bf2f(X2[off]);
+        tile[tl][tt] = h2f(X0[off]) + h2f(X1[off]);
     }
     __syncthreads();
 #pragma unroll
@@ -862,27 +826,20 @@
     float* NEG  = ws + NEG_F;
     unsigned short* HT0 = (unsigned short*)ws;
     unsigned short* HT1 = HT0 + 1280000;
-    unsigned short* HT2 = HT0 + 2560000;
     unsigned short* Fp0 = (unsigned short*)ws;
     unsigned short* Fp1 = Fp0 + 2560000;
-    unsigned short* Fp2 = Fp0 + 5120000;
     unsigned short* Gp0 = (unsigned short*)(ws + G_F);
     unsigned short* Gp1 = Gp0 + 2560000;
-    unsigned short* Gp2 = Gp0 + 5120000;
     unsigned short* H20 = (unsigned short*)ws;
     unsigned short* H21 = H20 + 5120000;
-    unsigned short* H22 = H20 + 10240000;
     unsigned short* TI0 = (unsigned short*)(ws + TI_F);
     unsigned short* CW0 = (unsigned short*)(ws + CW_F);
     unsigned short* X0 = (unsigned short*)(ws + X_F);
     unsigned short* X1 = X0 + 1280000;
-    unsigned short* X2 = X0 + 2560000;
     unsigned short* HF0 = (unsigned short*)(ws + HF_F);
     unsigned short* HF1 = HF0 + 1280000;
-    unsigned short* HF2b = HF0 + 2560000;
     unsigned short* W0 = (unsigned short*)(ws + W_F);
     unsigned short* W1 = W0 + 983040;
-    unsigned short* W2 = W0 + 1966080;
     float* SQ = ws + SQ_F;
     double* PART = (double*)(ws + PART_F);
     float* FIN = ws + FIN_F;
@@ -911,24 +868,24 @@
         case 3: {
             int psz = 2 * 10000 * 128;
             splitT_k<<<dim3(157, 2, 2), 256, 0, stream>>>(
-                cur, TI0, TI0 + psz, TI0 + 2 * psz, 128, 10000);
+                cur, TI0, TI0 + psz, 128, 10000);
             int tot = 256 * 1152;
             wconvp_k<<<(tot + 255) / 256, 256, 0, stream>>>(
-                swp[3], CW0, CW0 + tot, CW0 + 2 * tot, 128, tot);
-            mconv6p_k<128><<<dim3(40, 4, 2), 256, 0, stream>>>(
-                TI0, TI0 + psz, TI0 + 2 * psz, CW0, CW0 + tot, CW0 + 2 * tot,
+                swp[3], CW0, CW0 + tot, 128, tot);
+            mconv3h_k<128><<<dim3(40, 4, 2), 256, 0, stream>>>(
+                TI0, TI0 + psz, CW0, CW0 + tot,
                 sbp[3], outb, 256, 100, 100, 50, 50, 2);
             break;
         }
         case 4: {
             int psz = 2 * 2500 * 256;
             splitT_k<<<dim3(40, 4, 2), 256, 0, stream>>>(
-                cur, TI0, TI0 + psz, TI0 + 2 * psz, 256, 2500);
+                cur, TI0, TI0 + psz, 256, 2500);
             int tot = 256 * 2304;
             wconvp_k<<<(tot + 255) / 256, 256, 0, stream>>>(
-                swp[4], CW0, CW0 + tot, CW0 + 2 * tot, 256, tot);
-            mconv6p_k<256><<<dim3(40, 4, 2), 256, 0, stream>>>(
-                TI0, TI0 + psz, TI0 + 2 * psz, CW0, CW0 + tot, CW0 + 2 * tot,
+                swp[4], CW0, CW0 + tot, 256, tot);
+            mconv3h_k<256><<<dim3(40, 4, 2), 256, 0, stream>>>(
+                TI0, TI0 + psz, CW0, CW0 + tot,
                 sbp[4], outb, 256, 50, 50, 50, 50, 1);
             break;
         }
@@ -941,7 +898,7 @@
                                                             Co[l], HWo, cpg, (l < 4) ? 1 : 0, total);
         cur = outb;
     }
-    posadd_k<<<dim3(40, 4, 2), 256, 0, stream>>>(cur, X0, X1, X2);
+    posadd_k<<<dim3(40, 4, 2), 256, 0, stream>>>(cur, X0, X1);
 
     const int KS[12] = {9, 9, 10, 11, 12, 13, 13, 14, 15, 16, 17, 18};
     const int DILS[12] = {1, 1, 1, 1, 2, 2, 2, 2, 3, 3, 3, 3};
@@ -951,36 +908,36 @@
         pack5p_k<<<3840, 256, 0, stream>>>(
             fc1_w + (size_t)i * 65536, mr_w + (size_t)i * 262144,
             fc2_w + (size_t)i * 131072, ffn1_w + (size_t)i * 262144,
-            ffn2_w + (size_t)i * 262144, W0, W1, W2);
-
-        mgemm6p_k<2><<<dim3(40, 4, 2), 256, 0, stream>>>(
-            X0, X1, X2, W0, W1, W2,
+            ffn2_w + (size_t)i * 262144, W0, W1);
+
+        mgemm3h_k<2><<<dim3(40, 4, 2), 256, 0, stream>>>(
+            X0, X1, W0, W1,
             fc1_b + i * D, fc1_g + i * D, fc1_be + i * D,
-            nullptr, nullptr, nullptr, HF0, HF1, HF2b, N, D, D, 0);
-        tok_k<<<dim3(625, 2), 256, 0, stream>>>(HF0, HF1, HF2b, HT0, HT1, HT2, SQ);
+            nullptr, nullptr, HF0, HF1, N, D, D, 0);
+        tok_k<<<dim3(625, 2), 256, 0, stream>>>(HF0, HF1, HT0, HT1, SQ);
         for (int bz = 0; bz < 2; bz++) {
-            mdist6p_k<<<dim3(820, 1, 1), 256, 0, stream>>>(HT0, HT1, HT2, SQ, NEG, N, D, bz);
+            mdist3h_k<<<dim3(820, 1, 1), 256, 0, stream>>>(HT0, HT1, SQ, NEG, N, D, bz);
             topk_k<<<dim3(1250, 1, 1), 128, 0, stream>>>(NEG, IDX, N,
                                                          KS[i] * DILS[i], DILS[i], KS[i], bz);
         }
-        gather_k<<<dim3(2500, 2), 256, 0, stream>>>(HF0, HF1, HF2b, IDX, Fp0, Fp1, Fp2, KS[i]);
-        mgemm6p_k<4><<<dim3(40, 4, 2), 256, 0, stream>>>(
-            Fp0, Fp1, Fp2, W0 + 65536, W1 + 65536, W2 + 65536,
+        gather_k<<<dim3(2500, 2), 256, 0, stream>>>(HF0, HF1, IDX, Fp0, Fp1, KS[i]);
+        mgemm3h_k<4><<<dim3(40, 4, 2), 256, 0, stream>>>(
+            Fp0, Fp1, W0 + 65536, W1 + 65536,
             nullptr, mr_g + i * 512, mr_be + i * 512,
-            nullptr, nullptr, nullptr, Gp0, Gp1, Gp2, N, 512, 512, 1);
-        mgemm6p_k<2><<<dim3(40, 4, 2), 256, 0, stream>>>(
-            Gp0, Gp1, Gp2, W0 + 327680, W1 + 327680, W2 + 327680,
+            nullptr, nullptr, Gp0, Gp1, N, 512, 512, 1);
+        mgemm3h_k<2><<<dim3(40, 4, 2), 256, 0, stream>>>(
+            Gp0, Gp1, W0 + 327680, W1 + 327680,
             fc2_b + i * D, fc2_g + i * D, fc2_be + i * D,
-            X0, X1, X2, X0, X1, X2, N, D, 512, 0);
-        mgemm6p_k<4><<<dim3(40, 8, 2), 256, 0, stream>>>(
-            X0, X1, X2, W0 + 458752, W1 + 458752, W2 + 458752,
+            X0, X1, X0, X1, N, D, 512, 0);
+        mgemm3h_k<4><<<dim3(40, 8, 2), 256, 0, stream>>>(
+            X0, X1, W0 + 458752, W1 + 458752,
             ffn1_b + i * 1024, ffn1_g + i * 1024, ffn1_be + i * 1024,
-            nullptr, nullptr, nullptr, H20, H21, H22, N, 1024, D, 1);
-        mgemm6p_k<2><<<dim3(40, 4, 2), 256, 0, stream>>>(
-            H20, H21, H22, W0 + 720896, W1 + 720896, W2 + 720896,
+            nullptr, nullptr, H20, H21, N, 1024, D, 1);
+        mgemm3h_k<2><<<dim3(40, 4, 2), 256, 0, stream>>>(
+            H20, H21, W0 + 720896, W1 + 720896,
             ffn2_b + i * D, ffn2_g + i * D, ffn2_be + i * D,
-            X0, X1, X2, X0, X1, X2, N, D, 1024, 0);
-    }
-
-    outt_k<<<dim3(40, 4, 2), 256, 0, stream>>>(X0, X1, X2, (float*)d_out);
-}
+            X0, X1, X0, X1, N, D, 1024, 0);
+    }
+
+    outt_k<<<dim3(40, 4, 2), 256, 0, stream>>>(X0, X1, (float*)d_out);
+}
```

Result: faster. 3.672 ms (-16.3%).
